# Kernel optimization log

Measured on AMD Instinct MI355X. Metric: run time of the kernel, lower is better.

## Reference

```python
import jax, jax.numpy as jnp
import numpy as np

# H36M 17-joint skeleton: parent-of array
_PARENTS = [-1, 0, 1, 2, 0, 4, 5, 0, 7, 8, 9, 8, 11, 12, 8, 14, 15]

def _make_triplets():
    # (jp, j, jc) for every joint j with a parent jp and child jc
    trips = []
    for jc, j in enumerate(_PARENTS):
        if j <= 0 and j != 0:
            continue
        if j == -1:
            continue
        jp = _PARENTS[j]
        if jp == -1:
            continue
        trips.append((jp, j, jc))
    return trips

TRIPLETS = _make_triplets()  # 12 fixed triplets

B, N, J, C = 16, 243, 17, 512
H, D = 8, C // 8
EPS = 1e-5


def setup_inputs() -> dict:
    key = jax.random.key(0)
    ks = jax.random.split(key, 5)
    s = 1.0 / np.sqrt(C)
    x = jax.random.normal(ks[0], (B, N, J, C), dtype=jnp.float32)
    Wqkv = jax.random.normal(ks[1], (C, 3 * C), dtype=jnp.float32) * s
    bqkv = jax.random.normal(ks[2], (3 * C,), dtype=jnp.float32) * 0.01
    Wproj = jax.random.normal(ks[3], (C, C), dtype=jnp.float32) * s
    bproj = jax.random.normal(ks[4], (C,), dtype=jnp.float32) * 0.01
    return {"x": x, "Wqkv": Wqkv, "bqkv": bqkv, "Wproj": Wproj, "bproj": bproj}


def _hsdm(x, Wqkv, bqkv, Wproj, bproj):
    # x: (B, N, J, C) -> tokens over joints per frame
    xf = x.reshape(B * N, J, C)
    qkv = xf @ Wqkv + bqkv                                   # (BN, J, 3C)
    qkv = qkv.reshape(B * N, J, 3, H, D).transpose(2, 0, 3, 1, 4)  # (3, BN, H, J, D)
    q, k, v = qkv[0], qkv[1], qkv[2]
    scale = 1.0 / jnp.sqrt(jnp.float32(D))
    attn = jax.nn.softmax(jnp.einsum('bhqd,bhkd->bhqk', q, k) * scale, axis=-1)
    # sequential hierarchical adjustment over fixed skeleton triplets
    # (order matters: later triplets read entries written by earlier ones)
    for jp, j, jc in TRIPLETS:
        half = attn[:, :, j, jp] * 0.5
        attn = attn.at[:, :, j, jc].add(half).at[:, :, jc, j].add(half)
    # dropout is identity at inference
    xa = jnp.einsum('bhqk,bhkd->bhqd', attn, v)              # (BN, H, J, D)
    xa = xa.transpose(0, 2, 1, 3).reshape(B * N, J, C)
    xa = xa @ Wproj + bproj
    y = x + xa.reshape(B, N, J, C)
    mu = jnp.mean(y, axis=-1, keepdims=True)
    var = jnp.var(y, axis=-1, keepdims=True)
    return (y - mu) / jnp.sqrt(var + EPS)                     # LN without affine


def reference(x, Wqkv, bqkv, Wproj, bproj):
    return _hsdm(x, Wqkv, bqkv, Wproj, bproj)
```

## Files before the change

kernel.cpp:

```cpp
#include <hip/hip_runtime.h>

typedef unsigned short u16;
typedef unsigned int u32;
typedef short bf16x8 __attribute__((ext_vector_type(8)));
typedef float f32x4 __attribute__((ext_vector_type(4)));

#define M_ROWS   66096
#define M_PAD    66176
#define C_DIM    512
#define NQKV     1536
#define NFRAME   3888


__device__ __forceinline__ u16 f2bf(float f) {
    u32 u = __float_as_uint(f);
    u32 r = (u + 0x7fffu + ((u >> 16) & 1u)) >> 16;
    return (u16)r;
}
__device__ __forceinline__ float bf2f(u16 v) {
    return __uint_as_float(((u32)v) << 16);
}
__device__ __forceinline__ void async16(const void* g, void* l) {
    __builtin_amdgcn_global_load_lds(
        (const __attribute__((address_space(1))) unsigned int*)g,
        (__attribute__((address_space(3))) unsigned int*)l, 16, 0, 0);
}


__global__ __launch_bounds__(256) void cast_x(const float* __restrict__ x, u16* __restrict__ xb) {
    u32 cid = blockIdx.x * 256u + threadIdx.x;
    u32 m  = cid >> 6;
    u32 c0 = (cid & 63u) * 8u;
    if (m >= M_PAD) return;
    u16 v[8];
    if (m < M_ROWS) {
        const float* p = x + (size_t)m * C_DIM + c0;
        float4 f1 = *(const float4*)p;
        float4 f2 = *(const float4*)(p + 4);
        v[0]=f2bf(f1.x); v[1]=f2bf(f1.y); v[2]=f2bf(f1.z); v[3]=f2bf(f1.w);
        v[4]=f2bf(f2.x); v[5]=f2bf(f2.y); v[6]=f2bf(f2.z); v[7]=f2bf(f2.w);
    } else {
        #pragma unroll
        for (int i = 0; i < 8; ++i) v[i] = 0;
    }
    u16* dst = xb + ((size_t)(c0 >> 5) * M_PAD + m) * 32 + (c0 & 31u);
    *(uint4*)dst = *(const uint4*)v;
}


__global__ __launch_bounds__(256) void cast_w(const float* __restrict__ W, u16* __restrict__ out, int N) {
    __shared__ float tile[32 * 65];
    const int n0 = blockIdx.x * 64;
    const int kt = blockIdx.y;
    const int t  = threadIdx.x;
    for (int i = t; i < 2048; i += 256) {
        int k = i >> 6, n = i & 63;
        tile[k * 65 + n] = W[(size_t)(kt * 32 + k) * N + n0 + n];
    }
    __syncthreads();
    {
        int n = t >> 2, kk0 = (t & 3) * 8;
        u16 v[8];
        #pragma unroll
        for (int j = 0; j < 8; ++j) v[j] = f2bf(tile[(kk0 + j) * 65 + n]);
        u16* dst = out + ((size_t)kt * N + n0 + n) * 32 + kk0;
        *(uint4*)dst = *(const uint4*)v;
    }
}


__global__ __launch_bounds__(256) void gemm1(const u16* __restrict__ xb,
                                             const u16* __restrict__ wt,
                                             const float* __restrict__ bqkv,
                                             u16* __restrict__ qkv) {
    __shared__ u16 As[128 * 32];
    __shared__ u16 Bs[128 * 32];
    __shared__ float biasS[128];

    const int n0 = blockIdx.x * 128;
    const int m0 = blockIdx.y * 128;
    const int t  = threadIdx.x;
    const int w  = t >> 6, l = t & 63;
    const int lr = l & 15, lq = l >> 4;
    const int wr = (w >> 1) * 64, wc = (w & 1) * 64;

    if (t < 128) biasS[t] = bqkv[n0 + t];

    f32x4 acc[4][4] = {};

    for (int kt = 0; kt < 16; ++kt) {
        __syncthreads();
        const u16* ga = xb + ((size_t)kt * M_PAD + m0) * 32;
        const u16* gb = wt + ((size_t)kt * NQKV + n0) * 32;
        async16(ga + (size_t)t * 8,         &As[t * 8]);
        async16(ga + (size_t)(t + 256) * 8, &As[(t + 256) * 8]);
        async16(gb + (size_t)t * 8,         &Bs[t * 8]);
        async16(gb + (size_t)(t + 256) * 8, &Bs[(t + 256) * 8]);
        __syncthreads();

        bf16x8 a[4], b[4];
        #pragma unroll
        for (int i = 0; i < 4; ++i) a[i] = *(const bf16x8*)&As[(wr + i * 16 + lr) * 32 + lq * 8];
        #pragma unroll
        for (int i = 0; i < 4; ++i) b[i] = *(const bf16x8*)&Bs[(wc + i * 16 + lr) * 32 + lq * 8];
        #pragma unroll
        for (int i = 0; i < 4; ++i)
            #pragma unroll
            for (int j = 0; j < 4; ++j)
                acc[i][j] = __builtin_amdgcn_mfma_f32_16x16x32_bf16(a[i], b[j], acc[i][j], 0, 0, 0);
    }

    #pragma unroll
    for (int i = 0; i < 4; ++i) {
        #pragma unroll
        for (int j = 0; j < 4; ++j) {
            const int col  = n0 + wc + j * 16 + lr;
            const float bb = biasS[wc + j * 16 + lr];
            #pragma unroll
            for (int r = 0; r < 4; ++r) {
                const int row = m0 + wr + i * 16 + lq * 4 + r;
                if (row < M_ROWS)
                    qkv[(size_t)row * NQKV + col] = f2bf(acc[i][j][r] + bb);
            }
        }
    }
}


__constant__ int TRJP[13] = {0,1,0,4,0,7,8,7,8,11,7,8,14};
__constant__ int TRJ [13] = {1,2,4,5,7,8,9,8,11,12,8,14,15};
__constant__ int TRJC[13] = {2,3,5,6,8,9,10,11,12,13,14,15,16};

__device__ __forceinline__ float dot8(uint4 qa, uint4 kb) {
    const u32* qu = (const u32*)&qa;
    const u32* ku = (const u32*)&kb;
    float s = 0.f;
    #pragma unroll
    for (int i = 0; i < 4; ++i) {
        float q0 = __uint_as_float(qu[i] << 16);
        float q1 = __uint_as_float(qu[i] & 0xffff0000u);
        float k0 = __uint_as_float(ku[i] << 16);
        float k1 = __uint_as_float(ku[i] & 0xffff0000u);
        s = fmaf(q0, k0, s);
        s = fmaf(q1, k1, s);
    }
    return s;
}

#define QKROW 1552

__global__ __launch_bounds__(256) void attn_k(const u16* __restrict__ qkv, u16* __restrict__ xa) {
    __shared__ u16 qk[17 * QKROW];
    __shared__ float S[4][17 * 18];

    const int f = blockIdx.x;
    const int t = threadIdx.x;
    const int w = t >> 6, l = t & 63;
    const u16* src = qkv + (size_t)f * 17 * NQKV;

    for (int i = t; i < 3264; i += 256) {
        int r = i / 192, c = i - r * 192;
        *(uint4*)&qk[r * QKROW + c * 8] = *(const uint4*)&src[i * 8];
    }
    __syncthreads();

    for (int hh = 0; hh < 2; ++hh) {
        const int h = hh * 4 + w;
        float* Sw = S[w];

        for (int e = l; e < 289; e += 64) {
            int qi = e / 17, ki = e - qi * 17;
            const u16* qp = &qk[qi * QKROW + h * 64];
            const u16* kp = &qk[ki * QKROW + 512 + h * 64];
            float d = 0.f;
            #pragma unroll
            for (int c = 0; c < 8; ++c)
                d += dot8(*(const uint4*)&qp[c * 8], *(const uint4*)&kp[c * 8]);
            Sw[qi * 18 + ki] = d * 0.125f;
        }
        __syncthreads();

        if (l < 17) {
            float mx = -1e30f;
            #pragma unroll
            for (int k = 0; k < 17; ++k) mx = fmaxf(mx, Sw[l * 18 + k]);
            float s = 0.f;
            #pragma unroll
            for (int k = 0; k < 17; ++k) {
                float e = __expf(Sw[l * 18 + k] - mx);
                Sw[l * 18 + k] = e;
                s += e;
            }
            float inv = 1.f / s;
            #pragma unroll
            for (int k = 0; k < 17; ++k) Sw[l * 18 + k] *= inv;
        }
        __syncthreads();

        if (l == 0) {
            #pragma unroll
            for (int tr = 0; tr < 13; ++tr) {
                int jp = TRJP[tr], j = TRJ[tr], jc = TRJC[tr];
                float half = Sw[j * 18 + jp] * 0.5f;
                Sw[j * 18 + jc] += half;
                Sw[jc * 18 + j] += half;
            }
        }
        __syncthreads();

        float vreg[17];
        #pragma unroll
        for (int k = 0; k < 17; ++k) vreg[k] = bf2f(qk[k * QKROW + 1024 + h * 64 + l]);
        const int col = h * 64 + l;
        u16* dst = xa + ((size_t)(col >> 5) * M_PAD) * 32 + (col & 31);
        #pragma unroll
        for (int j = 0; j < 17; ++j) {
            float o = 0.f;
            #pragma unroll
            for (int k = 0; k < 17; ++k) o = fmaf(Sw[j * 18 + k], vreg[k], o);
            const int row = f * 17 + j;
            dst[(size_t)row * 32] = f2bf(o);
        }
        __syncthreads();
    }
}


__global__ __launch_bounds__(256) void gemm2_gemm(const u16* __restrict__ xa,
                                                  const u16* __restrict__ wt,
                                                  const float* __restrict__ bproj,
                                                  const float* __restrict__ x,
                                                  float* __restrict__ y) {
    __shared__ u16 As[128 * 32];
    __shared__ u16 Bs[128 * 32];
    __shared__ float biasS[128];

    const int n0 = blockIdx.x * 128;
    const int m0 = blockIdx.y * 128;
    const int t  = threadIdx.x;
    const int w  = t >> 6, l = t & 63;
    const int lr = l & 15, lq = l >> 4;
    const int wr = (w >> 1) * 64, wc = (w & 1) * 64;

    if (t < 128) biasS[t] = bproj[n0 + t];

    f32x4 acc[4][4] = {};

    for (int kt = 0; kt < 16; ++kt) {
        __syncthreads();
        const u16* ga = xa + ((size_t)kt * M_PAD + m0) * 32;
        const u16* gb = wt + ((size_t)kt * C_DIM + n0) * 32;
        async16(ga + (size_t)t * 8,         &As[t * 8]);
        async16(ga + (size_t)(t + 256) * 8, &As[(t + 256) * 8]);
        async16(gb + (size_t)t * 8,         &Bs[t * 8]);
        async16(gb + (size_t)(t + 256) * 8, &Bs[(t + 256) * 8]);
        __syncthreads();

        bf16x8 a[4], b[4];
        #pragma unroll
        for (int i = 0; i < 4; ++i) a[i] = *(const bf16x8*)&As[(wr + i * 16 + lr) * 32 + lq * 8];
        #pragma unroll
        for (int i = 0; i < 4; ++i) b[i] = *(const bf16x8*)&Bs[(wc + i * 16 + lr) * 32 + lq * 8];
        #pragma unroll
        for (int i = 0; i < 4; ++i)
            #pragma unroll
            for (int j = 0; j < 4; ++j)
                acc[i][j] = __builtin_amdgcn_mfma_f32_16x16x32_bf16(a[i], b[j], acc[i][j], 0, 0, 0);
    }

    #pragma unroll
    for (int i = 0; i < 4; ++i) {
        #pragma unroll
        for (int j = 0; j < 4; ++j) {
            const int col  = n0 + wc + j * 16 + lr;
            const float bb = biasS[wc + j * 16 + lr];
            #pragma unroll
            for (int r = 0; r < 4; ++r) {
                const int row = m0 + wr + i * 16 + lq * 4 + r;
                if (row < M_ROWS) {
                    const size_t idx = (size_t)row * C_DIM + col;
                    y[idx] = acc[i][j][r] + bb + x[idx];
                }
            }
        }
    }
}


__global__ __launch_bounds__(256) void ln_k(const float* __restrict__ y, float* __restrict__ out) {
    const int row = blockIdx.x * 4 + (threadIdx.x >> 6);
    const int l   = threadIdx.x & 63;
    const float* p = y + (size_t)row * C_DIM + l * 8;
    float4 a = *(const float4*)p;
    float4 b = *(const float4*)(p + 4);
    float s  = a.x + a.y + a.z + a.w + b.x + b.y + b.z + b.w;
    float sq = a.x*a.x + a.y*a.y + a.z*a.z + a.w*a.w
             + b.x*b.x + b.y*b.y + b.z*b.z + b.w*b.w;
    #pragma unroll
    for (int m = 1; m < 64; m <<= 1) {
        s  += __shfl_xor(s, m);
        sq += __shfl_xor(sq, m);
    }
    const float mean = s * (1.f / 512.f);
    const float var  = sq * (1.f / 512.f) - mean * mean;
    const float rstd = rsqrtf(var + 1e-5f);
    float* q = out + (size_t)row * C_DIM + l * 8;
    float4 o1, o2;
    o1.x = (a.x - mean) * rstd; o1.y = (a.y - mean) * rstd;
    o1.z = (a.z - mean) * rstd; o1.w = (a.w - mean) * rstd;
    o2.x = (b.x - mean) * rstd; o2.y = (b.y - mean) * rstd;
    o2.z = (b.z - mean) * rstd; o2.w = (b.w - mean) * rstd;
    *(float4*)q = o1;
    *(float4*)(q + 4) = o2;
}


extern "C" void kernel_launch(void* const* d_in, const int* in_sizes, int n_in,
                              void* d_out, int out_size, void* d_ws, size_t ws_size,
                              hipStream_t stream) {
    const float* x     = (const float*)d_in[0];
    const float* Wqkv  = (const float*)d_in[1];
    const float* bqkv  = (const float*)d_in[2];
    const float* Wproj = (const float*)d_in[3];
    const float* bproj = (const float*)d_in[4];
    float* out = (float*)d_out;

    u16* xb  = (u16*)d_ws;
    u16* wqt = xb  + (size_t)M_PAD * C_DIM;
    u16* wpt = wqt + (size_t)NQKV * C_DIM;
    u16* qkv = wpt + (size_t)C_DIM * C_DIM;
    u16* xa  = qkv + (size_t)M_PAD * NQKV;
    float* y = (float*)qkv;

    cast_x<<<(M_PAD * 64) / 256, 256, 0, stream>>>(x, xb);
    cast_w<<<dim3(NQKV / 64, 16), 256, 0, stream>>>(Wqkv, wqt, NQKV);
    cast_w<<<dim3(C_DIM / 64, 16), 256, 0, stream>>>(Wproj, wpt, C_DIM);
    gemm1<<<dim3(NQKV / 128, M_PAD / 128), 256, 0, stream>>>(xb, wqt, bqkv, qkv);
    attn_k<<<NFRAME, 256, 0, stream>>>(qkv, xa);
    gemm2_gemm<<<dim3(C_DIM / 128, M_PAD / 128), 256, 0, stream>>>(xa, wpt, bproj, x, y);
    ln_k<<<M_ROWS / 4, 256, 0, stream>>>(y, out);
}
```

Measured before the change: 743.8 us.

## Rewrite attention kernel to use MFMA per (frame, head) wavefront

The attention kernel now assigns one wavefront per (frame, head) pair instead of one block per frame. It computes QK^T and PV with 32x32x16 bf16 MFMA instructions loaded directly from global memory, does softmax with cross-lane shuffles, and applies the skeleton triplet adjustments through lane shuffles. P is staged through a small per-wave LDS tile in bf16. This removes the scalar dot products, the block-wide syncs and the single-lane triplet loop. In exchange it pads 17 joints up to 32, rounds P to bf16 before the PV product, and gathers V with strided scalar loads.

```diff
diff --git a/kernel.cpp b/kernel.cpp
--- a/kernel.cpp
+++ b/kernel.cpp
@@ -4,6 +4,7 @@
 typedef unsigned int u32;
 typedef short bf16x8 __attribute__((ext_vector_type(8)));
 typedef float f32x4 __attribute__((ext_vector_type(4)));
+typedef float f32x16 __attribute__((ext_vector_type(16)));
 
 #define M_ROWS   66096
 #define M_PAD    66176
@@ -127,101 +128,102 @@
 }
 
 
-__constant__ int TRJP[13] = {0,1,0,4,0,7,8,7,8,11,7,8,14};
-__constant__ int TRJ [13] = {1,2,4,5,7,8,9,8,11,12,8,14,15};
-__constant__ int TRJC[13] = {2,3,5,6,8,9,10,11,12,13,14,15,16};
-
-__device__ __forceinline__ float dot8(uint4 qa, uint4 kb) {
-    const u32* qu = (const u32*)&qa;
-    const u32* ku = (const u32*)&kb;
-    float s = 0.f;
-    #pragma unroll
-    for (int i = 0; i < 4; ++i) {
-        float q0 = __uint_as_float(qu[i] << 16);
-        float q1 = __uint_as_float(qu[i] & 0xffff0000u);
-        float k0 = __uint_as_float(ku[i] << 16);
-        float k1 = __uint_as_float(ku[i] & 0xffff0000u);
-        s = fmaf(q0, k0, s);
-        s = fmaf(q1, k1, s);
-    }
-    return s;
-}
-
-#define QKROW 1552
-
 __global__ __launch_bounds__(256) void attn_k(const u16* __restrict__ qkv, u16* __restrict__ xa) {
-    __shared__ u16 qk[17 * QKROW];
-    __shared__ float S[4][17 * 18];
-
-    const int f = blockIdx.x;
-    const int t = threadIdx.x;
-    const int w = t >> 6, l = t & 63;
-    const u16* src = qkv + (size_t)f * 17 * NQKV;
-
-    for (int i = t; i < 3264; i += 256) {
-        int r = i / 192, c = i - r * 192;
-        *(uint4*)&qk[r * QKROW + c * 8] = *(const uint4*)&src[i * 8];
-    }
-    __syncthreads();
-
-    for (int hh = 0; hh < 2; ++hh) {
-        const int h = hh * 4 + w;
-        float* Sw = S[w];
-
-        for (int e = l; e < 289; e += 64) {
-            int qi = e / 17, ki = e - qi * 17;
-            const u16* qp = &qk[qi * QKROW + h * 64];
-            const u16* kp = &qk[ki * QKROW + 512 + h * 64];
-            float d = 0.f;
-            #pragma unroll
-            for (int c = 0; c < 8; ++c)
-                d += dot8(*(const uint4*)&qp[c * 8], *(const uint4*)&kp[c * 8]);
-            Sw[qi * 18 + ki] = d * 0.125f;
-        }
-        __syncthreads();
-
-        if (l < 17) {
-            float mx = -1e30f;
-            #pragma unroll
-            for (int k = 0; k < 17; ++k) mx = fmaxf(mx, Sw[l * 18 + k]);
-            float s = 0.f;
-            #pragma unroll
-            for (int k = 0; k < 17; ++k) {
-                float e = __expf(Sw[l * 18 + k] - mx);
-                Sw[l * 18 + k] = e;
-                s += e;
+    __shared__ u16 Pb[4][32 * 40];
+
+    const int wv  = threadIdx.x >> 6;
+    const int l   = threadIdx.x & 63;
+    const int l31 = l & 31;
+    const int hi  = l >> 5;
+
+    const int id = blockIdx.x * 4 + wv;
+    const int f  = id >> 3;
+    const int h  = id & 7;
+
+    const int mrow = (l31 < 17) ? l31 : 0;
+    const u16* base = qkv + (size_t)(f * 17) * NQKV;
+    const u16* Qp = base + (size_t)mrow * NQKV + h * 64 + 8 * hi;
+    const u16* Kp = Qp + 512;
+
+    f32x16 Sacc = {};
+    #pragma unroll
+    for (int c = 0; c < 4; ++c) {
+        bf16x8 aq = *(const bf16x8*)(Qp + 16 * c);
+        bf16x8 bk = *(const bf16x8*)(Kp + 16 * c);
+        Sacc = __builtin_amdgcn_mfma_f32_32x32x16_bf16(aq, bk, Sacc, 0, 0, 0);
+    }
+
+    float p[16];
+    #pragma unroll
+    for (int r = 0; r < 16; ++r)
+        p[r] = (l31 < 17) ? Sacc[r] * 0.125f : -1e30f;
+
+    #pragma unroll
+    for (int r = 0; r < 16; ++r) {
+        float mx = p[r];
+        #pragma unroll
+        for (int m = 1; m < 32; m <<= 1) mx = fmaxf(mx, __shfl_xor(mx, m));
+        float e = __expf(p[r] - mx);
+        float s = e;
+        #pragma unroll
+        for (int m = 1; m < 32; m <<= 1) s += __shfl_xor(s, m);
+        p[r] = e * __builtin_amdgcn_rcpf(s);
+    }
+
+    {
+        constexpr int TJP[13] = {0,1,0,4,0,7,8,7,8,11,7,8,14};
+        constexpr int TJ [13] = {1,2,4,5,7,8,9,8,11,12,8,14,15};
+        constexpr int TJC[13] = {2,3,5,6,8,9,10,11,12,13,14,15,16};
+        #pragma unroll
+        for (int tr = 0; tr < 13; ++tr) {
+            const int jp = TJP[tr], j = TJ[tr], jc = TJC[tr];
+            const int rj = (j  & 3) | ((j  >> 3) << 2), hj = (j  >> 2) & 1;
+            const int rc = (jc & 3) | ((jc >> 3) << 2), hc = (jc >> 2) & 1;
+            const float half = 0.5f * __shfl(p[rj], jp + 32 * hj);
+            if (l == jc + 32 * hj) p[rj] += half;
+            if (l == j  + 32 * hc) p[rc] += half;
+        }
+    }
+
+    u16* Pw = Pb[wv];
+    #pragma unroll
+    for (int r = 0; r < 16; ++r) {
+        const int row = (r & 3) + 8 * (r >> 2) + 4 * hi;
+        Pw[row * 40 + l31] = f2bf(p[r]);
+    }
+    asm volatile("s_waitcnt lgkmcnt(0)" ::: "memory");
+
+    bf16x8 pa[2];
+    #pragma unroll
+    for (int c = 0; c < 2; ++c)
+        pa[c] = *(const bf16x8*)&Pw[l31 * 40 + 16 * c + 8 * hi];
+
+    const u16* Vbase = base + 1024 + h * 64;
+    f32x16 O[2] = {};
+    #pragma unroll
+    for (int t = 0; t < 2; ++t) {
+        #pragma unroll
+        for (int c = 0; c < 2; ++c) {
+            u16 vv[8];
+            #pragma unroll
+            for (int j = 0; j < 8; ++j) {
+                const int k  = 16 * c + 8 * hi + j;
+                const int kr = (k < 17) ? k : 0;
+                vv[j] = Vbase[(size_t)kr * NQKV + t * 32 + l31];
             }
-            float inv = 1.f / s;
-            #pragma unroll
-            for (int k = 0; k < 17; ++k) Sw[l * 18 + k] *= inv;
-        }
-        __syncthreads();
-
-        if (l == 0) {
-            #pragma unroll
-            for (int tr = 0; tr < 13; ++tr) {
-                int jp = TRJP[tr], j = TRJ[tr], jc = TRJC[tr];
-                float half = Sw[j * 18 + jp] * 0.5f;
-                Sw[j * 18 + jc] += half;
-                Sw[jc * 18 + j] += half;
-            }
-        }
-        __syncthreads();
-
-        float vreg[17];
-        #pragma unroll
-        for (int k = 0; k < 17; ++k) vreg[k] = bf2f(qk[k * QKROW + 1024 + h * 64 + l]);
-        const int col = h * 64 + l;
-        u16* dst = xa + ((size_t)(col >> 5) * M_PAD) * 32 + (col & 31);
-        #pragma unroll
-        for (int j = 0; j < 17; ++j) {
-            float o = 0.f;
-            #pragma unroll
-            for (int k = 0; k < 17; ++k) o = fmaf(Sw[j * 18 + k], vreg[k], o);
-            const int row = f * 17 + j;
-            dst[(size_t)row * 32] = f2bf(o);
-        }
-        __syncthreads();
+            O[t] = __builtin_amdgcn_mfma_f32_32x32x16_bf16(pa[c], *(const bf16x8*)vv, O[t], 0, 0, 0);
+        }
+    }
+
+    #pragma unroll
+    for (int t = 0; t < 2; ++t) {
+        const int kt = h * 2 + t;
+        #pragma unroll
+        for (int r = 0; r < 16; ++r) {
+            const int row = (r & 3) + 8 * (r >> 2) + 4 * hi;
+            if (row < 17)
+                xa[((size_t)kt * M_PAD + (f * 17 + row)) * 32 + l31] = f2bf(O[t][r]);
+        }
     }
 }
 
@@ -336,7 +338,7 @@
     cast_w<<<dim3(NQKV / 64, 16), 256, 0, stream>>>(Wqkv, wqt, NQKV);
     cast_w<<<dim3(C_DIM / 64, 16), 256, 0, stream>>>(Wproj, wpt, C_DIM);
     gemm1<<<dim3(NQKV / 128, M_PAD / 128), 256, 0, stream>>>(xb, wqt, bqkv, qkv);
-    attn_k<<<NFRAME, 256, 0, stream>>>(qkv, xa);
+    attn_k<<<(NFRAME * 8) / 4, 256, 0, stream>>>(qkv, xa);
     gemm2_gemm<<<dim3(C_DIM / 128, M_PAD / 128), 256, 0, stream>>>(xa, wpt, bproj, x, y);
     ln_k<<<M_ROWS / 4, 256, 0, stream>>>(y, out);
 }
```

New measurement: 657.0 us. 11.7% less time.
